# Performance work log

Measured on AMD Instinct MI355X. Metric: run time of the kernel, lower is better.

## Reference

```python
import jax, jax.numpy as jnp
import numpy as np

B_, S_, E_ = 1, 2048, 2048
NH, P_, N_, G_, K_, CS = 64, 64, 128, 1, 4, 256
INTER = NH * P_            # 4096
CONV_DIM = INTER + 2 * G_ * N_  # 4352
PROJ = INTER + CONV_DIM + NH
EPS = 1e-5


def setup_inputs() -> dict:
    key = jax.random.key(0)
    ks = jax.random.split(key, 6)
    return {
        "input_states": jax.random.normal(ks[0], (B_, S_, E_), dtype=jnp.float32),
        "mask": jnp.ones((B_, 1, S_), dtype=jnp.int32),
        "W_in": jax.random.normal(ks[1], (PROJ, E_), dtype=jnp.float32) * 0.02,
        "conv_w": jax.random.normal(ks[2], (CONV_DIM, K_), dtype=jnp.float32) * 0.2,
        "conv_b": jnp.zeros((CONV_DIM,), dtype=jnp.float32),
        "dt_bias": jnp.ones((NH,), dtype=jnp.float32),
        "A_log": jnp.log(jnp.arange(1, NH + 1, dtype=jnp.float32)),
        "D": jnp.ones((NH,), dtype=jnp.float32),
        "norm_w": jnp.ones((INTER,), dtype=jnp.float32),
        "W_out": jax.random.normal(ks[3], (E_, INTER), dtype=jnp.float32) * 0.02,
    }


def segsum(x):
    # x: [..., L]; out[..., i, j] = sum_{j < k <= i} x[..., k], -inf above diagonal
    L = x.shape[-1]
    i = jnp.arange(L)
    strict = i[:, None] > i[None, :]
    X = jnp.where(strict, x[..., :, None], 0.0)   # [..., L(i), L(j)]
    S = jnp.cumsum(X, axis=-2)
    return jnp.where(i[:, None] >= i[None, :], S, -jnp.inf)


def reference(input_states, mask, W_in, conv_w, conv_b, dt_bias, A_log, D, norm_w, W_out):
    B, S, E = input_states.shape
    # mask has shape[1]==1 -> apply_mask_to_padding_states is a no-op
    proj = input_states @ W_in.T                      # [B,S,PROJ]
    gate = proj[..., :INTER]
    h_BC = proj[..., INTER:INTER + CONV_DIM]
    dt = proj[..., INTER + CONV_DIM:]                 # [B,S,NH]

    # causal depthwise conv1d (padding=K-1, truncated to seq_len)
    xpad = jnp.pad(h_BC, ((0, 0), (K_ - 1, 0), (0, 0)))
    conv = conv_b
    for i in range(K_):
        conv = conv + xpad[:, i:i + S, :] * conv_w[:, i]
    h_BC = jax.nn.silu(conv)

    hidden = h_BC[..., :INTER]
    Bm = h_BC[..., INTER:INTER + G_ * N_]
    Cm = h_BC[..., INTER + G_ * N_:]

    A = -jnp.exp(A_log)                               # [NH]
    dt = jnp.clip(jax.nn.softplus(dt + dt_bias), 0.0) # [B,S,NH]

    Hs = hidden.reshape(B, S, NH, P_).astype(jnp.float32)
    Bm = jnp.tile(Bm.reshape(B, S, G_, N_).astype(jnp.float32), (1, 1, NH // G_, 1))
    Cm = jnp.tile(Cm.reshape(B, S, G_, N_).astype(jnp.float32), (1, 1, NH // G_, 1))

    D_resid = D[None, None, :, None] * Hs             # pad=0 since S % CS == 0
    Hdt = Hs * dt[..., None]
    At = A * dt                                       # [B,S,NH]

    C_ = S // CS
    Hc = Hdt.reshape(B, C_, CS, NH, P_)
    Ac = At.reshape(B, C_, CS, NH)
    Bc = Bm.reshape(B, C_, CS, NH, N_)
    Cc = Cm.reshape(B, C_, CS, NH, N_)

    Ap = jnp.transpose(Ac, (0, 3, 1, 2))              # [B,H,C,L]
    A_cum = jnp.cumsum(Ap, axis=-1)                   # [B,H,C,L]
    L_tri = jnp.exp(segsum(Ap))                       # [B,H,C,L,L]

    # diagonal (intra-chunk) output
    Gm = jnp.einsum('bclhn,bcshn->bclsh', Cc, Bc)
    M = Gm * jnp.transpose(L_tri, (0, 2, 3, 4, 1))    # [B,C,L,S,H]
    Yd = jnp.einsum('bclsh,bcshp->bclhp', M, Hc)

    # per-chunk states (note: source uses same-chunk states, no inter-chunk scan)
    decay = jnp.exp(A_cum[..., -1:] - A_cum)          # [B,H,C,L]
    Bd = Bc * jnp.transpose(decay, (0, 2, 3, 1))[..., None]
    states = jnp.einsum('bclhn,bclhp->bchpn', Bd, Hc) # [B,C,H,P,N]

    Sd = jnp.transpose(jnp.exp(A_cum), (0, 2, 3, 1))  # [B,C,L,H]
    Yoff = jnp.einsum('bclhn,bchpn->bclhp', Cc, states) * Sd[..., None]

    y = (Yd + Yoff).reshape(B, S, NH, P_) + D_resid
    y = y.reshape(B, S, INTER)

    # gated RMSNorm (fp32)
    yf = y.astype(jnp.float32) * jax.nn.silu(gate.astype(jnp.float32))
    var = jnp.mean(yf * yf, axis=-1, keepdims=True)
    yn = norm_w * (yf * jax.lax.rsqrt(var + EPS))

    return yn @ W_out.T
```

## Files before the change

kernel.cpp:

```cpp
#include <hip/hip_runtime.h>
#include <math.h>

#define S_LEN   2048
#define E_DIM   2048
#define NH      64
#define P_DIM   64
#define N_DIM   128
#define CS      256
#define NCHUNK  8
#define INTER   4096
#define CONVD   4352
#define PROJ    8512
#define GEMM1N  8448
#define EPS     1e-5f

#define OFF_PROJBF 0ull
#define OFF_HBC    8650752ull
#define OFF_DTG    13107200ull
#define OFF_DTPART 13238272ull
#define OFF_GM     17432576ull
#define OFF_YV     17956864ull
#define OFF_R      26345472ull

typedef __bf16 bf16x8 __attribute__((ext_vector_type(8)));
typedef float  f32x4  __attribute__((ext_vector_type(4)));
typedef float  f32x16 __attribute__((ext_vector_type(16)));

__device__ __forceinline__ float bf2f(unsigned short u) {
    union { unsigned int i; float f; } v; v.i = ((unsigned int)u) << 16; return v.f;
}
__device__ __forceinline__ unsigned short f2bf(float f) {
    union { float f; unsigned int i; } v; v.f = f;
    unsigned int r = v.i + 0x7FFFu + ((v.i >> 16) & 1u);
    return (unsigned short)(r >> 16);
}
__device__ __forceinline__ void gl_lds16(const void* g, void* l) {
    __builtin_amdgcn_global_load_lds(
        (const __attribute__((address_space(1))) void*)g,
        (__attribute__((address_space(3))) void*)l, 16, 0, 0);
}

__global__ __launch_bounds__(256) void cast_bf16_kernel(
    const float* __restrict__ in, unsigned short* __restrict__ out)
{
    size_t i = ((size_t)blockIdx.x * 256 + threadIdx.x) * 8;
    float4 a = *(const float4*)(in + i);
    float4 b = *(const float4*)(in + i + 4);
    uint4 o;
    o.x = (unsigned int)f2bf(a.x) | ((unsigned int)f2bf(a.y) << 16);
    o.y = (unsigned int)f2bf(a.z) | ((unsigned int)f2bf(a.w) << 16);
    o.z = (unsigned int)f2bf(b.x) | ((unsigned int)f2bf(b.y) << 16);
    o.w = (unsigned int)f2bf(b.z) | ((unsigned int)f2bf(b.w) << 16);
    *(uint4*)(out + i) = o;
}

__global__ __launch_bounds__(256) void gemm_bt_mfma(
    const unsigned short* __restrict__ A, int lda, long long sA,
    const unsigned short* __restrict__ B, int ldb, long long sB,
    float* __restrict__ Cf, unsigned short* __restrict__ Cb, int ldc,
    long long sC, int K)
{
    __shared__ unsigned short As[128 * 64];
    __shared__ unsigned short Bs[128 * 64];
    A += (long long)blockIdx.z * sA;
    B += (long long)blockIdx.z * sB;
    const int t     = threadIdx.x;
    const int m0    = blockIdx.y * 128;
    const int n0    = blockIdx.x * 128;
    const int w     = t >> 6;
    const int lane  = t & 63;
    const int col   = lane & 31;
    const int khalf = lane >> 5;
    const int wm    = (w & 1) * 64;
    const int wn    = (w >> 1) * 64;

    const int srow  = t >> 3;
    const int sslot = t & 7;
    const unsigned short* Agp[4];
    const unsigned short* Bgp[4];
#pragma unroll
    for (int i = 0; i < 4; i++) {
        const int r   = srow + 32 * i;
        const int gch = sslot ^ ((r ^ (r >> 3)) & 7);
        Agp[i] = A + (size_t)(m0 + r) * lda + gch * 8;
        Bgp[i] = B + (size_t)(n0 + r) * ldb + gch * 8;
    }
    unsigned short* Asl = &As[t * 8];
    unsigned short* Bsl = &Bs[t * 8];

    int aOff[2], aXor[2], bOff[2], bXor[2];
#pragma unroll
    for (int i = 0; i < 2; i++) {
        const int ra = wm + i * 32 + col;
        aOff[i] = ra * 64; aXor[i] = (ra ^ (ra >> 3)) & 7;
        const int rb = wn + i * 32 + col;
        bOff[i] = rb * 64; bXor[i] = (rb ^ (rb >> 3)) & 7;
    }

    f32x16 acc[2][2];
#pragma unroll
    for (int mi = 0; mi < 2; mi++)
#pragma unroll
        for (int ni = 0; ni < 2; ni++)
#pragma unroll
            for (int e = 0; e < 16; e++) acc[mi][ni][e] = 0.f;

    for (int k0 = 0; k0 < K; k0 += 64) {
        __syncthreads();
#pragma unroll
        for (int i = 0; i < 4; i++) {
            gl_lds16(Agp[i] + k0, Asl + i * 2048);
            gl_lds16(Bgp[i] + k0, Bsl + i * 2048);
        }
        __syncthreads();
#pragma unroll
        for (int ks = 0; ks < 4; ks++) {
            const int ch = ks * 2 + khalf;
            bf16x8 af[2], bfr[2];
#pragma unroll
            for (int i = 0; i < 2; i++) {
                af[i]  = *(const bf16x8*)&As[aOff[i] + ((ch ^ aXor[i]) * 8)];
                bfr[i] = *(const bf16x8*)&Bs[bOff[i] + ((ch ^ bXor[i]) * 8)];
            }
#pragma unroll
            for (int mi = 0; mi < 2; mi++)
#pragma unroll
                for (int ni = 0; ni < 2; ni++)
                    acc[mi][ni] = __builtin_amdgcn_mfma_f32_32x32x16_bf16(
                        af[mi], bfr[ni], acc[mi][ni], 0, 0, 0);
        }
    }

    if (Cb) {
#pragma unroll
        for (int mi = 0; mi < 2; mi++)
#pragma unroll
            for (int ni = 0; ni < 2; ni++) {
                const int rbase = m0 + wm + mi * 32 + 4 * khalf;
                const int cc    = n0 + wn + ni * 32 + col;
#pragma unroll
                for (int g = 0; g < 4; g++)
#pragma unroll
                    for (int rr = 0; rr < 4; rr++)
                        Cb[(size_t)(rbase + 8 * g + rr) * ldc + cc] =
                            f2bf(acc[mi][ni][4 * g + rr]);
            }
    } else {
        float* Cz = Cf + (long long)blockIdx.z * sC;
#pragma unroll
        for (int mi = 0; mi < 2; mi++)
#pragma unroll
            for (int ni = 0; ni < 2; ni++) {
                const int rbase = m0 + wm + mi * 32 + 4 * khalf;
                const int cc    = n0 + wn + ni * 32 + col;
#pragma unroll
                for (int g = 0; g < 4; g++)
#pragma unroll
                    for (int rr = 0; rr < 4; rr++)
                        Cz[(size_t)(rbase + 8 * g + rr) * ldc + cc] =
                            acc[mi][ni][4 * g + rr];
            }
    }
}

__global__ __launch_bounds__(256) void addf_kernel(
    const float* __restrict__ a, const float* __restrict__ b,
    float* __restrict__ o)
{
    size_t i = ((size_t)blockIdx.x * 256 + threadIdx.x) * 4;
    float4 x = *(const float4*)(a + i);
    float4 y = *(const float4*)(b + i);
    float4 r = make_float4(x.x + y.x, x.y + y.y, x.z + y.z, x.w + y.w);
    *(float4*)(o + i) = r;
}

__global__ __launch_bounds__(256) void gemm_nt(
    const float* __restrict__ A, int lda, long long sA,
    const float* __restrict__ B, int ldb, long long sB,
    float* __restrict__ C, int ldc, long long sC, int K)
{
    A += (long long)blockIdx.z * sA;
    B += (long long)blockIdx.z * sB;
    C += (long long)blockIdx.z * sC;
    const int t  = threadIdx.x;
    const int m0 = blockIdx.y * 128;
    const int n0 = blockIdx.x * 64;
    __shared__ float As[16][132];
    __shared__ float Bs[16][68];
    const int tx = t & 15;
    const int ty = t >> 4;

    const int arow = t & 127;
    const int akh  = (t >> 7) * 8;
    const float* Aload = A + (size_t)(m0 + arow) * (size_t)lda + akh;
    const int brow = t & 63;
    const int bk4  = (t >> 6) * 4;
    const float* Bload = B + (size_t)(n0 + brow) * (size_t)ldb + bk4;

    float acc[8][4];
#pragma unroll
    for (int i = 0; i < 8; i++)
#pragma unroll
        for (int j = 0; j < 4; j++) acc[i][j] = 0.f;

    for (int k0 = 0; k0 < K; k0 += 16) {
        __syncthreads();
        float4 a0 = *(const float4*)(Aload + k0);
        float4 a1 = *(const float4*)(Aload + k0 + 4);
        float4 b0 = *(const float4*)(Bload + k0);
        As[akh + 0][arow] = a0.x; As[akh + 1][arow] = a0.y;
        As[akh + 2][arow] = a0.z; As[akh + 3][arow] = a0.w;
        As[akh + 4][arow] = a1.x; As[akh + 5][arow] = a1.y;
        As[akh + 6][arow] = a1.z; As[akh + 7][arow] = a1.w;
        Bs[bk4 + 0][brow] = b0.x; Bs[bk4 + 1][brow] = b0.y;
        Bs[bk4 + 2][brow] = b0.z; Bs[bk4 + 3][brow] = b0.w;
        __syncthreads();
#pragma unroll
        for (int k = 0; k < 16; k++) {
            float4 a4 = *(const float4*)(&As[k][ty * 8]);
            float4 a5 = *(const float4*)(&As[k][ty * 8 + 4]);
            float4 b4 = *(const float4*)(&Bs[k][tx * 4]);
            float am[8] = {a4.x, a4.y, a4.z, a4.w, a5.x, a5.y, a5.z, a5.w};
            float bn[4] = {b4.x, b4.y, b4.z, b4.w};
#pragma unroll
            for (int i = 0; i < 8; i++)
#pragma unroll
                for (int j = 0; j < 4; j++) acc[i][j] += am[i] * bn[j];
        }
    }
#pragma unroll
    for (int i = 0; i < 8; i++) {
        float4 o = make_float4(acc[i][0], acc[i][1], acc[i][2], acc[i][3]);
        *(float4*)(C + (size_t)(m0 + ty * 8 + i) * (size_t)ldc + n0 + tx * 4) = o;
    }
}

__global__ __launch_bounds__(256) void dt_reduce_kernel(
    const float* __restrict__ part, const float* __restrict__ dt_bias,
    float* __restrict__ dtg)
{
    const int i = blockIdx.x * 256 + threadIdx.x;
    float x = dt_bias[i & 63];
#pragma unroll
    for (int z = 0; z < 32; z++) x += part[(size_t)z * 131072 + i];
    dtg[i] = (x > 20.f) ? x : log1pf(__expf(x));
}

__global__ __launch_bounds__(256) void conv_silu8_kernel(
    const unsigned short* __restrict__ projbf, const float* __restrict__ conv_w,
    const float* __restrict__ conv_b, unsigned short* __restrict__ out)
{
    const int c  = blockIdx.x * 256 + threadIdx.x;
    const int s0 = blockIdx.y * 8;
    const float4 w = *(const float4*)(conv_w + (size_t)c * 4);
    const float b = conv_b[c];
    const size_t base = 4096 + (size_t)c;
    float v[11];
#pragma unroll
    for (int m = 0; m < 11; m++) {
        int s = s0 - 3 + m;
        v[m] = (s >= 0) ? bf2f(projbf[(size_t)s * GEMM1N + base]) : 0.f;
    }
#pragma unroll
    for (int j = 0; j < 8; j++) {
        float acc = b + v[j] * w.x + v[j + 1] * w.y + v[j + 2] * w.z + v[j + 3] * w.w;
        float sig = 1.f / (1.f + __expf(-acc));
        out[(size_t)(s0 + j) * CONVD + c] = f2bf(acc * sig);
    }
}

__global__ __launch_bounds__(256, 2) void ssm_mfma_kernel(
    const unsigned short* __restrict__ hBC, const float* __restrict__ dtg,
    const float* __restrict__ Gm, const float* __restrict__ A_log,
    const float* __restrict__ Dp, float* __restrict__ y)
{
    const int h    = blockIdx.x;
    const int c    = blockIdx.y;
    const int t    = threadIdx.x;
    const int wid  = t >> 6;
    const int lane = t & 63;
    const int lo   = lane & 15;
    const int q    = lane >> 4;

    __shared__ float sAcum[CS], sdt[CS], sD[CS], sEs[CS], sDecay[CS], sScl[CS];
    __shared__ float sWaveSum[4];
    __shared__ unsigned short sHdtT[64 * 264];
    __shared__ unsigned short sStT[64 * 136];
    __shared__ unsigned short sBufB[128 * 72];

    const float A = -__expf(A_log[h]);
    const int row0 = c * CS;
    const unsigned short* hid = hBC + (size_t)row0 * CONVD + h * P_DIM;
    const unsigned short* Bp  = hBC + (size_t)row0 * CONVD + INTER;
    const unsigned short* Cp  = hBC + (size_t)row0 * CONVD + INTER + N_DIM;
    const float* gm = Gm + (size_t)c * CS * CS;

    float dtv = dtg[(size_t)(row0 + t) * NH + h];
    float v = A * dtv;
    for (int off = 1; off < 64; off <<= 1) {
        float u = __shfl_up(v, off, 64);
        if (lane >= off) v += u;
    }
    if (lane == 63) sWaveSum[wid] = v;
    __syncthreads();
    float pre = 0.f;
    for (int i = 0; i < 4; i++) if (i < wid) pre += sWaveSum[i];
    v += pre;
    sAcum[t] = v;
    sdt[t] = dtv;
    __syncthreads();
    const float AcumEnd = sAcum[CS - 1];
    {
        float ac   = sAcum[t];
        float apre = (t < 64) ? 0.f : sAcum[(t & ~63) - 1];
        sD[t]     = __expf(ac - apre);
        sEs[t]    = __expf(sAcum[t | 63] - ac);
        sDecay[t] = __expf(AcumEnd - ac);
        sScl[t]   = __expf(ac);
    }

    unsigned short* stgu = sStT;
    for (int lt = 0; lt < 4; lt++) {
        __syncthreads();
        {
            const int c8 = (t & 7) * 8;
#pragma unroll
            for (int j = 0; j < 2; j++) {
                int l = (t >> 3) + 32 * j;
                *(uint4*)&stgu[l * 64 + c8] =
                    *(const uint4*)(hid + (size_t)(lt * 64 + l) * CONVD + c8);
            }
        }
        __syncthreads();
        {
            const int p = t & 63, lq = (t >> 6) * 16;
#pragma unroll
            for (int j = 0; j < 4; j++) {
                ushort4 pk;
                int l0 = lq + j * 4;
                pk.x = f2bf(bf2f(stgu[(l0 + 0) * 64 + p]) * sdt[lt * 64 + l0 + 0]);
                pk.y = f2bf(bf2f(stgu[(l0 + 1) * 64 + p]) * sdt[lt * 64 + l0 + 1]);
                pk.z = f2bf(bf2f(stgu[(l0 + 2) * 64 + p]) * sdt[lt * 64 + l0 + 2]);
                pk.w = f2bf(bf2f(stgu[(l0 + 3) * 64 + p]) * sdt[lt * 64 + l0 + 3]);
                *(uint2*)&sHdtT[p * 264 + lt * 64 + l0] = *(uint2*)&pk;
            }
        }
    }

    f32x4 acc2[2][4];
#pragma unroll
    for (int mi = 0; mi < 2; mi++)
#pragma unroll
        for (int ni = 0; ni < 4; ni++) acc2[mi][ni] = (f32x4){0.f, 0.f, 0.f, 0.f};
    const int psub = (wid & 1) * 32;
    const int nsub = (wid >> 1) * 64;

    for (int qt = 0; qt < 4; qt++) {
        for (int hf = 0; hf < 2; hf++) {
            __syncthreads();
            {
                const int n8 = (t & 15) * 8;
#pragma unroll
                for (int j = 0; j < 2; j++) {
                    int r = (t >> 4) + 16 * j;
                    *(uint4*)&stgu[r * 128 + n8] =
                        *(const uint4*)(Bp + (size_t)(qt * 64 + hf * 32 + r) * CONVD + n8);
                }
            }
            __syncthreads();
            {
                const int n = t & 127, lc = (t >> 7) * 16;
#pragma unroll
                for (int j = 0; j < 4; j++) {
                    int l0 = lc + j * 4;
                    ushort4 pk;
                    pk.x = f2bf(bf2f(stgu[(l0 + 0) * 128 + n]) * sDecay[qt * 64 + hf * 32 + l0 + 0]);
                    pk.y = f2bf(bf2f(stgu[(l0 + 1) * 128 + n]) * sDecay[qt * 64 + hf * 32 + l0 + 1]);
                    pk.z = f2bf(bf2f(stgu[(l0 + 2) * 128 + n]) * sDecay[qt * 64 + hf * 32 + l0 + 2]);
                    pk.w = f2bf(bf2f(stgu[(l0 + 3) * 128 + n]) * sDecay[qt * 64 + hf * 32 + l0 + 3]);
                    *(uint2*)&sBufB[n * 72 + hf * 32 + l0] = *(uint2*)&pk;
                }
            }
        }
        __syncthreads();
#pragma unroll
        for (int ks = 0; ks < 2; ks++) {
            const int k0 = qt * 64 + ks * 32;
            const int kq = ks * 32;
            bf16x8 a2[2], b2[4];
#pragma unroll
            for (int mi = 0; mi < 2; mi++)
                a2[mi] = *(const bf16x8*)&sHdtT[(psub + mi * 16 + lo) * 264 + k0 + q * 8];
#pragma unroll
            for (int ni = 0; ni < 4; ni++)
                b2[ni] = *(const bf16x8*)&sBufB[(nsub + ni * 16 + lo) * 72 + kq + q * 8];
#pragma unroll
            for (int mi = 0; mi < 2; mi++)
#pragma unroll
                for (int ni = 0; ni < 4; ni++)
                    acc2[mi][ni] = __builtin_amdgcn_mfma_f32_16x16x32_bf16(
                        a2[mi], b2[ni], acc2[mi][ni], 0, 0, 0);
        }
    }
    __syncthreads();
#pragma unroll
    for (int mi = 0; mi < 2; mi++)
#pragma unroll
        for (int ni = 0; ni < 4; ni++)
#pragma unroll
            for (int rr = 0; rr < 4; rr++) {
                int p = psub + mi * 16 + q * 4 + rr;
                int n = nsub + ni * 16 + lo;
                sStT[p * 136 + n] = f2bf(acc2[mi][ni][rr]);
            }

    f32x4 accY[4][2][2];
#pragma unroll
    for (int i = 0; i < 4; i++)
#pragma unroll
        for (int mi = 0; mi < 2; mi++)
#pragma unroll
            for (int pi = 0; pi < 2; pi++) accY[i][mi][pi] = (f32x4){0.f, 0.f, 0.f, 0.f};
    const int pcol = (wid & 1) * 32;
    const int rsub = (wid >> 1) * 16;
    unsigned short* Cs = sBufB;

    for (int i = 0; i < 4; i++) {
        __syncthreads();
        {
            const int n8 = (t & 15) * 8;
#pragma unroll
            for (int j = 0; j < 4; j++) {
                int r = (t >> 4) + 16 * j;
                uint4 cv = *(const uint4*)(Cp + (size_t)(i * 64 + r) * CONVD + n8);
                float scl = sScl[i * 64 + r];
                const unsigned short* cu = (const unsigned short*)&cv;
                ushort4 p0, p1;
                p0.x = f2bf(bf2f(cu[0]) * scl); p0.y = f2bf(bf2f(cu[1]) * scl);
                p0.z = f2bf(bf2f(cu[2]) * scl); p0.w = f2bf(bf2f(cu[3]) * scl);
                p1.x = f2bf(bf2f(cu[4]) * scl); p1.y = f2bf(bf2f(cu[5]) * scl);
                p1.z = f2bf(bf2f(cu[6]) * scl); p1.w = f2bf(bf2f(cu[7]) * scl);
                *(uint2*)&Cs[r * 136 + n8]     = *(uint2*)&p0;
                *(uint2*)&Cs[r * 136 + n8 + 4] = *(uint2*)&p1;
            }
        }
        __syncthreads();
#pragma unroll
        for (int ks = 0; ks < 4; ks++) {
            const int k0 = ks * 32;
            bf16x8 a3[2], b3[2];
#pragma unroll
            for (int mi = 0; mi < 2; mi++)
                a3[mi] = *(const bf16x8*)&Cs[(mi * 32 + rsub + lo) * 136 + k0 + q * 8];
#pragma unroll
            for (int pi = 0; pi < 2; pi++)
                b3[pi] = *(const bf16x8*)&sStT[(pcol + pi * 16 + lo) * 136 + k0 + q * 8];
#pragma unroll
            for (int mi = 0; mi < 2; mi++)
#pragma unroll
                for (int pi = 0; pi < 2; pi++)
                    accY[i][mi][pi] = __builtin_amdgcn_mfma_f32_16x16x32_bf16(
                        a3[mi], b3[pi], accY[i][mi][pi], 0, 0, 0);
        }
    }

    unsigned short* Mt = sBufB;
    for (int i = 0; i < 4; i++) {
        const int nk = 2 * (i + 1);
        for (int mi = 0; mi < 2; mi++) {
            __syncthreads();
            if (wid <= i) {
                float P = 1.f;
                for (int m = wid + 1; m <= i - 1; m++) P *= sD[m * 64 + 63];
                const int s4 = wid * 64 + lo * 4;
                float4 es4 = *(const float4*)&sEs[s4];
#pragma unroll
                for (int j = 0; j < 8; j++) {
                    int lr = q + j * 4;
                    int l  = i * 64 + mi * 32 + lr;
                    float4 g4 = *(const float4*)&gm[(size_t)l * CS + s4];
                    float w0, w1, w2, w3;
                    if (wid == i) {
                        float al = sAcum[l];
                        w0 = (s4 + 0 <= l) ? __expf(al - sAcum[s4 + 0]) : 0.f;
                        w1 = (s4 + 1 <= l) ? __expf(al - sAcum[s4 + 1]) : 0.f;
                        w2 = (s4 + 2 <= l) ? __expf(al - sAcum[s4 + 2]) : 0.f;
                        w3 = (s4 + 3 <= l) ? __expf(al - sAcum[s4 + 3]) : 0.f;
                    } else {
                        float rs = sD[l] * P;
                        w0 = rs * es4.x; w1 = rs * es4.y;
                        w2 = rs * es4.z; w3 = rs * es4.w;
                    }
                    ushort4 pk;
                    pk.x = f2bf(g4.x * w0); pk.y = f2bf(g4.y * w1);
                    pk.z = f2bf(g4.z * w2); pk.w = f2bf(g4.w * w3);
                    *(uint2*)&Mt[lr * 264 + s4] = *(uint2*)&pk;
                }
            }
            __syncthreads();
            for (int ks = 0; ks < nk; ks++) {
                const int k0 = ks * 32;
                bf16x8 am = *(const bf16x8*)&Mt[(rsub + lo) * 264 + k0 + q * 8];
                bf16x8 b1[2];
#pragma unroll
                for (int pi = 0; pi < 2; pi++)
                    b1[pi] = *(const bf16x8*)&sHdtT[(pcol + pi * 16 + lo) * 264 + k0 + q * 8];
#pragma unroll
                for (int pi = 0; pi < 2; pi++)
                    accY[i][mi][pi] = __builtin_amdgcn_mfma_f32_16x16x32_bf16(
                        am, b1[pi], accY[i][mi][pi], 0, 0, 0);
            }
        }
    }

    const float Dh = Dp[h];
#pragma unroll
    for (int i = 0; i < 4; i++)
#pragma unroll
        for (int mi = 0; mi < 2; mi++)
#pragma unroll
            for (int pi = 0; pi < 2; pi++)
#pragma unroll
                for (int rr = 0; rr < 4; rr++) {
                    int l = i * 64 + mi * 32 + rsub + q * 4 + rr;
                    int p = pcol + pi * 16 + lo;
                    float hv = bf2f(hid[(size_t)l * CONVD + p]);
                    y[(size_t)(row0 + l) * INTER + h * P_DIM + p] =
                        accY[i][mi][pi][rr] + Dh * hv;
                }
}

__global__ __launch_bounds__(256) void norm_kernel(
    const float* __restrict__ y, const unsigned short* __restrict__ projbf,
    const float* __restrict__ norm_w, unsigned short* __restrict__ yn)
{
    const int s = blockIdx.x;
    const int t = threadIdx.x;
    __shared__ float sYf[INTER];
    __shared__ float sW[4];
    const float* yrow = y + (size_t)s * INTER;
    const unsigned short* grow = projbf + (size_t)s * GEMM1N;
    float sum = 0.f;
    for (int j0 = 0; j0 < INTER; j0 += 2048) {
        int j = j0 + t * 8;
        float4 y0 = *(const float4*)(yrow + j);
        float4 y1 = *(const float4*)(yrow + j + 4);
        uint4 gp = *(const uint4*)(grow + j);
        float gv[8] = {
            bf2f((unsigned short)(gp.x & 0xffff)), bf2f((unsigned short)(gp.x >> 16)),
            bf2f((unsigned short)(gp.y & 0xffff)), bf2f((unsigned short)(gp.y >> 16)),
            bf2f((unsigned short)(gp.z & 0xffff)), bf2f((unsigned short)(gp.z >> 16)),
            bf2f((unsigned short)(gp.w & 0xffff)), bf2f((unsigned short)(gp.w >> 16))};
        float yv8[8] = {y0.x, y0.y, y0.z, y0.w, y1.x, y1.y, y1.z, y1.w};
#pragma unroll
        for (int e = 0; e < 8; e++) {
            float f = yv8[e] * (gv[e] / (1.f + __expf(-gv[e])));
            sum += f * f;
            sYf[j + e] = f;
        }
    }
    for (int off = 32; off > 0; off >>= 1) sum += __shfl_down(sum, off, 64);
    if ((t & 63) == 0) sW[t >> 6] = sum;
    __syncthreads();
    const float var = (sW[0] + sW[1] + sW[2] + sW[3]) * (1.f / (float)INTER);
    const float rs = rsqrtf(var + EPS);
    for (int j0 = 0; j0 < INTER; j0 += 2048) {
        int j = j0 + t * 8;
        float4 w0 = *(const float4*)(norm_w + j);
        float4 w1 = *(const float4*)(norm_w + j + 4);
        float wv[8] = {w0.x, w0.y, w0.z, w0.w, w1.x, w1.y, w1.z, w1.w};
        unsigned short o[8];
#pragma unroll
        for (int e = 0; e < 8; e++) o[e] = f2bf(sYf[j + e] * wv[e] * rs);
        uint4 ov;
        ov.x = (unsigned int)o[0] | ((unsigned int)o[1] << 16);
        ov.y = (unsigned int)o[2] | ((unsigned int)o[3] << 16);
        ov.z = (unsigned int)o[4] | ((unsigned int)o[5] << 16);
        ov.w = (unsigned int)o[6] | ((unsigned int)o[7] << 16);
        *(uint4*)(yn + (size_t)s * INTER + j) = ov;
    }
}

extern "C" void kernel_launch(void* const* d_in, const int* in_sizes, int n_in,
                              void* d_out, int out_size, void* d_ws, size_t ws_size,
                              hipStream_t stream)
{
    const float* X       = (const float*)d_in[0];
    const float* W_in    = (const float*)d_in[2];
    const float* conv_w  = (const float*)d_in[3];
    const float* conv_b  = (const float*)d_in[4];
    const float* dt_bias = (const float*)d_in[5];
    const float* A_log   = (const float*)d_in[6];
    const float* Dp      = (const float*)d_in[7];
    const float* norm_w  = (const float*)d_in[8];
    const float* W_out   = (const float*)d_in[9];
    float* out = (float*)d_out;
    float* ws  = (float*)d_ws;

    unsigned short* projbf = (unsigned short*)(ws + OFF_PROJBF);
    unsigned short* hbc16  = (unsigned short*)(ws + OFF_HBC);
    float* dtg     = ws + OFF_DTG;
    float* dtpart  = ws + OFF_DTPART;
    float* gm      = ws + OFF_GM;
    float* yv      = ws + OFF_YV;
    unsigned short* Xbf    = (unsigned short*)(ws + OFF_R);
    unsigned short* Winbf  = (unsigned short*)(ws + OFF_R + 2097152);
    unsigned short* ynbf   = (unsigned short*)(ws + OFF_R);
    unsigned short* Woutbf = (unsigned short*)(ws + OFF_R + 4194304);
    float* part0 = ws + OFF_PROJBF;
    float* part1 = part0 + 4194304;

    cast_bf16_kernel<<<2048, 256, 0, stream>>>(X, Xbf);
    cast_bf16_kernel<<<8448, 256, 0, stream>>>(W_in, Winbf);

    gemm_bt_mfma<<<dim3(GEMM1N / 128, S_LEN / 128, 1), 256, 0, stream>>>(
        Xbf, E_DIM, 0LL, Winbf, E_DIM, 0LL, nullptr, projbf, GEMM1N, 0LL, E_DIM);

    cast_bf16_kernel<<<4096, 256, 0, stream>>>(W_out, Woutbf);

    gemm_nt<<<dim3(1, 16, 32), 256, 0, stream>>>(
        X, E_DIM, 64LL, W_in + (size_t)GEMM1N * E_DIM, E_DIM, 64LL,
        dtpart, NH, 131072LL, 64);
    dt_reduce_kernel<<<512, 256, 0, stream>>>(dtpart, dt_bias, dtg);

    conv_silu8_kernel<<<dim3(CONVD / 256, S_LEN / 8), 256, 0, stream>>>(
        projbf, conv_w, conv_b, hbc16);

    gemm_bt_mfma<<<dim3(CS / 128, CS / 128, NCHUNK), 256, 0, stream>>>(
        hbc16 + INTER + N_DIM, CONVD, (long long)CS * CONVD,
        hbc16 + INTER,         CONVD, (long long)CS * CONVD,
        gm, nullptr, CS, (long long)CS * CS, N_DIM);

    ssm_mfma_kernel<<<dim3(NH, NCHUNK), 256, 0, stream>>>(
        hbc16, dtg, gm, A_log, Dp, yv);

    norm_kernel<<<dim3(S_LEN), 256, 0, stream>>>(yv, projbf, norm_w, ynbf);

    gemm_bt_mfma<<<dim3(E_DIM / 128, S_LEN / 128, 2), 256, 0, stream>>>(
        ynbf, INTER, 2048LL, Woutbf, INTER, 2048LL,
        part0, nullptr, E_DIM, 4194304LL, 2048);
    addf_kernel<<<4096, 256, 0, stream>>>(part0, part1, out);
}
```

Baseline: 424.4 us.

## Merge casts into one kernel, swap GEMM1 grid order, split-K by four for out-proj

Replaces the three separate fp32-to-bf16 cast launches with one kernel that picks its source by block index, and moves the W_out copy to its own workspace region so it can be cast up front. The input-projection GEMM grid is transposed through a new mswap flag, so consecutive blocks walk along M and share the same W_in tile, which is meant to improve cache reuse. The output projection goes from split-K of 2 to split-K of 4, raising the block count from 512 to 1024 for better occupancy. This adds a 4-way partial-sum reduction with more fp32 partial traffic and needs a larger workspace.

```diff
diff --git a/kernel.cpp b/kernel.cpp
--- a/kernel.cpp
+++ b/kernel.cpp
@@ -21,6 +21,7 @@
 #define OFF_GM     17432576ull
 #define OFF_YV     17956864ull
 #define OFF_R      26345472ull
+#define OFF_WOUT   37093376ull
 
 typedef __bf16 bf16x8 __attribute__((ext_vector_type(8)));
 typedef float  f32x4  __attribute__((ext_vector_type(4)));
@@ -40,33 +41,40 @@
         (__attribute__((address_space(3))) void*)l, 16, 0, 0);
 }
 
-__global__ __launch_bounds__(256) void cast_bf16_kernel(
-    const float* __restrict__ in, unsigned short* __restrict__ out)
-{
-    size_t i = ((size_t)blockIdx.x * 256 + threadIdx.x) * 8;
-    float4 a = *(const float4*)(in + i);
-    float4 b = *(const float4*)(in + i + 4);
+__global__ __launch_bounds__(256) void cast3_kernel(
+    const float* __restrict__ X, const float* __restrict__ Win,
+    const float* __restrict__ Wout, unsigned short* __restrict__ Xbf,
+    unsigned short* __restrict__ Winbf, unsigned short* __restrict__ Woutbf)
+{
+    const int blk = blockIdx.x;
+    const float* src; unsigned short* dst; size_t off;
+    if (blk < 2048)       { src = X;    dst = Xbf;    off = (size_t)blk * 2048; }
+    else if (blk < 10496) { src = Win;  dst = Winbf;  off = (size_t)(blk - 2048) * 2048; }
+    else                  { src = Wout; dst = Woutbf; off = (size_t)(blk - 10496) * 2048; }
+    size_t i = off + (size_t)threadIdx.x * 8;
+    float4 a = *(const float4*)(src + i);
+    float4 b = *(const float4*)(src + i + 4);
     uint4 o;
     o.x = (unsigned int)f2bf(a.x) | ((unsigned int)f2bf(a.y) << 16);
     o.y = (unsigned int)f2bf(a.z) | ((unsigned int)f2bf(a.w) << 16);
     o.z = (unsigned int)f2bf(b.x) | ((unsigned int)f2bf(b.y) << 16);
     o.w = (unsigned int)f2bf(b.z) | ((unsigned int)f2bf(b.w) << 16);
-    *(uint4*)(out + i) = o;
+    *(uint4*)(dst + i) = o;
 }
 
 __global__ __launch_bounds__(256) void gemm_bt_mfma(
     const unsigned short* __restrict__ A, int lda, long long sA,
     const unsigned short* __restrict__ B, int ldb, long long sB,
     float* __restrict__ Cf, unsigned short* __restrict__ Cb, int ldc,
-    long long sC, int K)
+    long long sC, int K, int mswap)
 {
     __shared__ unsigned short As[128 * 64];
     __shared__ unsigned short Bs[128 * 64];
     A += (long long)blockIdx.z * sA;
     B += (long long)blockIdx.z * sB;
     const int t     = threadIdx.x;
-    const int m0    = blockIdx.y * 128;
-    const int n0    = blockIdx.x * 128;
+    const int m0    = (mswap ? blockIdx.x : blockIdx.y) * 128;
+    const int n0    = (mswap ? blockIdx.y : blockIdx.x) * 128;
     const int w     = t >> 6;
     const int lane  = t & 63;
     const int col   = lane & 31;
@@ -163,14 +171,16 @@
     }
 }
 
-__global__ __launch_bounds__(256) void addf_kernel(
-    const float* __restrict__ a, const float* __restrict__ b,
-    float* __restrict__ o)
+__global__ __launch_bounds__(256) void addf4_kernel(
+    const float* __restrict__ p, float* __restrict__ o)
 {
     size_t i = ((size_t)blockIdx.x * 256 + threadIdx.x) * 4;
-    float4 x = *(const float4*)(a + i);
-    float4 y = *(const float4*)(b + i);
-    float4 r = make_float4(x.x + y.x, x.y + y.y, x.z + y.z, x.w + y.w);
+    float4 a = *(const float4*)(p + i);
+    float4 b = *(const float4*)(p + i + 4194304);
+    float4 c = *(const float4*)(p + i + 8388608);
+    float4 d = *(const float4*)(p + i + 12582912);
+    float4 r = make_float4(a.x + b.x + c.x + d.x, a.y + b.y + c.y + d.y,
+                           a.z + b.z + c.z + d.z, a.w + b.w + c.w + d.w);
     *(float4*)(o + i) = r;
 }
 
@@ -606,17 +616,14 @@
     unsigned short* Xbf    = (unsigned short*)(ws + OFF_R);
     unsigned short* Winbf  = (unsigned short*)(ws + OFF_R + 2097152);
     unsigned short* ynbf   = (unsigned short*)(ws + OFF_R);
-    unsigned short* Woutbf = (unsigned short*)(ws + OFF_R + 4194304);
-    float* part0 = ws + OFF_PROJBF;
-    float* part1 = part0 + 4194304;
-
-    cast_bf16_kernel<<<2048, 256, 0, stream>>>(X, Xbf);
-    cast_bf16_kernel<<<8448, 256, 0, stream>>>(W_in, Winbf);
-
-    gemm_bt_mfma<<<dim3(GEMM1N / 128, S_LEN / 128, 1), 256, 0, stream>>>(
-        Xbf, E_DIM, 0LL, Winbf, E_DIM, 0LL, nullptr, projbf, GEMM1N, 0LL, E_DIM);
-
-    cast_bf16_kernel<<<4096, 256, 0, stream>>>(W_out, Woutbf);
+    unsigned short* Woutbf = (unsigned short*)(ws + OFF_WOUT);
+    float* part = ws;
+
+    cast3_kernel<<<14592, 256, 0, stream>>>(X, W_in, W_out, Xbf, Winbf, Woutbf);
+
+    gemm_bt_mfma<<<dim3(S_LEN / 128, GEMM1N / 128, 1), 256, 0, stream>>>(
+        Xbf, E_DIM, 0LL, Winbf, E_DIM, 0LL, nullptr, projbf, GEMM1N, 0LL,
+        E_DIM, 1);
 
     gemm_nt<<<dim3(1, 16, 32), 256, 0, stream>>>(
         X, E_DIM, 64LL, W_in + (size_t)GEMM1N * E_DIM, E_DIM, 64LL,
@@ -629,15 +636,15 @@
     gemm_bt_mfma<<<dim3(CS / 128, CS / 128, NCHUNK), 256, 0, stream>>>(
         hbc16 + INTER + N_DIM, CONVD, (long long)CS * CONVD,
         hbc16 + INTER,         CONVD, (long long)CS * CONVD,
-        gm, nullptr, CS, (long long)CS * CS, N_DIM);
+        gm, nullptr, CS, (long long)CS * CS, N_DIM, 0);
 
     ssm_mfma_kernel<<<dim3(NH, NCHUNK), 256, 0, stream>>>(
         hbc16, dtg, gm, A_log, Dp, yv);
 
     norm_kernel<<<dim3(S_LEN), 256, 0, stream>>>(yv, projbf, norm_w, ynbf);
 
-    gemm_bt_mfma<<<dim3(E_DIM / 128, S_LEN / 128, 2), 256, 0, stream>>>(
-        ynbf, INTER, 2048LL, Woutbf, INTER, 2048LL,
-        part0, nullptr, E_DIM, 4194304LL, 2048);
-    addf_kernel<<<4096, 256, 0, stream>>>(part0, part1, out);
-}
+    gemm_bt_mfma<<<dim3(E_DIM / 128, S_LEN / 128, 4), 256, 0, stream>>>(
+        ynbf, INTER, 1024LL, Woutbf, INTER, 1024LL,
+        part, nullptr, E_DIM, 4194304LL, 1024, 0);
+    addf4_kernel<<<4096, 256, 0, stream>>>(part, out);
+}
```

Result: no change. 421.6 us (-0.7%).
